# Kernel tuning notes

Hardware: AMD Instinct MI355X
Metric: run time of the kernel (lower is better)

The kernel has to match this reference:

```python
import jax, jax.numpy as jnp
import numpy as np
from jax import lax

DIM = 384
NH = 8
HD = DIM // NH
M = 16          # num_anchors
B = 16
HH = 64
WW = 64
N = HH * WW
STD = 0.02


def setup_inputs() -> dict:
    key = jax.random.key(0)
    ks = jax.random.split(key, 12)
    rn = lambda k, shape: (jax.random.normal(k, shape, jnp.float32) * STD)
    return {
        "x": jax.random.normal(ks[0], (B, N, DIM), jnp.float32),
        "H": HH,
        "W": WW,
        "saliency_w": rn(ks[1], (DIM, 1)),
        "saliency_b": jnp.zeros((1,), jnp.float32),
        "anchor_seeds": rn(ks[2], (1, M, DIM)),
        "w_q_agg": rn(ks[3], (DIM, DIM)),
        "w_kv_agg": rn(ks[4], (DIM, 2 * DIM)),
        "w_q_self": rn(ks[5], (DIM, DIM)),
        "w_kv_self": rn(ks[6], (DIM, 2 * DIM)),
        "w_q_bcast": rn(ks[7], (DIM, DIM)),
        "w_kv_bcast": rn(ks[8], (DIM, 2 * DIM)),
        "dw_kernel": rn(ks[9], (DIM, 1, 3, 3)),  # depthwise conv, OIHW with I=1
        "w_proj": rn(ks[10], (DIM, DIM)),
    }


def _mhsa(q_in, kv_in, wq, wkv):
    """Multi-head cross attention. q_in: [B,Lq,C], kv_in: [B,Lk,C]."""
    b, lq, c = q_in.shape
    lk = kv_in.shape[1]
    scale = HD ** -0.5
    q = (q_in @ wq).reshape(b, lq, NH, HD)
    kv = (kv_in @ wkv).reshape(b, lk, 2, NH, HD)
    k, v = kv[:, :, 0], kv[:, :, 1]
    attn = jnp.einsum("bqhd,bkhd->bhqk", q, k) * scale
    attn = jax.nn.softmax(attn, axis=-1)
    out = jnp.einsum("bhqk,bkhd->bqhd", attn, v).reshape(b, lq, c)
    return out


def reference(x, H, W, saliency_w, saliency_b, anchor_seeds,
              w_q_agg, w_kv_agg, w_q_self, w_kv_self,
              w_q_bcast, w_kv_bcast, dw_kernel, w_proj):
    b, n, c = x.shape
    # saliency gating
    sal = jax.nn.sigmoid(x @ saliency_w + saliency_b)  # [B,N,1]
    x_sal = x * sal
    # stage 1: anchors aggregate from saliency-gated tokens
    anchors = jnp.broadcast_to(anchor_seeds, (b, M, c))
    anchors = anchors + _mhsa(anchors, x_sal, w_q_agg, w_kv_agg)
    # stage 2: anchor self-attention
    anchors = anchors + _mhsa(anchors, anchors, w_q_self, w_kv_self)
    # stage 3: broadcast anchors back to all tokens
    global_out = _mhsa(x, anchors, w_q_bcast, w_kv_bcast)
    # depthwise 3x3 conv on the 2D token map
    x2d = x.reshape(b, H, W, c).transpose(0, 3, 1, 2)  # NCHW
    local = lax.conv_general_dilated(
        x2d, dw_kernel, window_strides=(1, 1), padding="SAME",
        feature_group_count=c,
        dimension_numbers=("NCHW", "OIHW", "NCHW"))
    local = local.transpose(0, 2, 3, 1).reshape(b, n, c)
    return (global_out + local) @ w_proj
```

## Files before the change

### kernel.cpp

```cpp
#include <hip/hip_runtime.h>
#include <hip/hip_bf16.h>

#define SCALE 0.14433756729740643f

typedef __attribute__((ext_vector_type(8))) short bf16x8;
typedef __attribute__((ext_vector_type(4))) float f32x4;

template <typename T> __device__ inline T cvt_from_f(float v);
template <> __device__ inline float cvt_from_f<float>(float v) { return v; }
template <> __device__ inline __hip_bfloat16 cvt_from_f<__hip_bfloat16>(float v) { return __float2bfloat16(v); }

__device__ inline void gload16(const void* g, void* l) {
  __builtin_amdgcn_global_load_lds((const __attribute__((address_space(1))) void*)g,
                                   (__attribute__((address_space(3))) void*)l, 16, 0, 0);
}

__device__ inline int xcd_flat(int nwg) {
  int flat = (blockIdx.z * gridDim.y + blockIdx.y) * gridDim.x + blockIdx.x;
  int per = nwg >> 3;
  return (flat & 7) * per + (flat >> 3);
}

__global__ __launch_bounds__(256) void prep(const float* __restrict__ x,
                                            const float* __restrict__ wsal,
                                            const float* __restrict__ bsal,
                                            __hip_bfloat16* __restrict__ xb,
                                            float* __restrict__ sal) {
  int wave = threadIdx.x >> 6, lane = threadIdx.x & 63;
  size_t row = (size_t)blockIdx.x * 4 + wave;
  const float* xr = x + row * 384;
  float xs[6];
  float part = 0.f;
#pragma unroll
  for (int j = 0; j < 6; j++) {
    int c = lane + 64 * j;
    xs[j] = xr[c];
    part += xs[j] * wsal[c];
  }
#pragma unroll
  for (int off = 32; off >= 1; off >>= 1) part += __shfl_xor(part, off);
  float s = 1.f / (1.f + __expf(-(part + bsal[0])));
#pragma unroll
  for (int j = 0; j < 6; j++) {
    int c = lane + 64 * j;
    xb[row * 384 + c] = __float2bfloat16(xs[j]);
  }
  if (lane == 0) sal[row] = s;
}

__global__ void wcast_tv(const float* __restrict__ w, __hip_bfloat16* __restrict__ wt) {
  int idx = blockIdx.x * 256 + threadIdx.x;
  if (idx >= 384 * 384) return;
  int n = idx / 384, k = idx % 384;
  wt[idx] = __float2bfloat16(w[(size_t)k * 768 + 384 + n]);
}

template <int K, typename OT, int BSHIFT>
__global__ __launch_bounds__(256) void gemm_mfma(const __hip_bfloat16* __restrict__ A,
                                                 const __hip_bfloat16* __restrict__ BT,
                                                 OT* __restrict__ out, int Ncols,
                                                 size_t btBatchStride) {
  __shared__ __align__(16) __hip_bfloat16 Asl[128][32];
  __shared__ __align__(16) __hip_bfloat16 Bsl[128][32];
  int nf = xcd_flat(gridDim.x * gridDim.y);
  int bX = nf % gridDim.x, bY = nf / gridDim.x;
  int tid = threadIdx.x;
  int lane = tid & 63;
  int w = tid >> 6;
  int wr = w >> 1, wc = w & 1;
  int fr = lane & 15, fq = lane >> 4;
  int rowBase = bY * 128, colBase = bX * 128;
  const __hip_bfloat16* BTb = BT + (size_t)(rowBase >> BSHIFT) * btBatchStride;

  int r1 = tid >> 2, kc1 = tid & 3;
  int r2 = (tid + 256) >> 2;

  char* aB1 = (char*)Asl + (size_t)(w * 64) * 16;
  char* aB2 = (char*)Asl + (size_t)(256 + w * 64) * 16;
  char* bB1 = (char*)Bsl + (size_t)(w * 64) * 16;
  char* bB2 = (char*)Bsl + (size_t)(256 + w * 64) * 16;

  const __hip_bfloat16* a1 = A + (size_t)(rowBase + r1) * K + kc1 * 8;
  const __hip_bfloat16* a2 = A + (size_t)(rowBase + r2) * K + kc1 * 8;
  const __hip_bfloat16* b1 = BTb + (size_t)(colBase + r1) * K + kc1 * 8;
  const __hip_bfloat16* b2 = BTb + (size_t)(colBase + r2) * K + kc1 * 8;

  f32x4 acc[4][4] = {};

  for (int kk = 0; kk < K; kk += 32) {
    gload16(a1 + kk, aB1);
    gload16(a2 + kk, aB2);
    gload16(b1 + kk, bB1);
    gload16(b2 + kk, bB2);
    __syncthreads();
    bf16x8 af[4], bfv[4];
#pragma unroll
    for (int m = 0; m < 4; m++) af[m] = *(const bf16x8*)&Asl[wr * 64 + m * 16 + fr][fq * 8];
#pragma unroll
    for (int n = 0; n < 4; n++) bfv[n] = *(const bf16x8*)&Bsl[wc * 64 + n * 16 + fr][fq * 8];
#pragma unroll
    for (int m = 0; m < 4; m++)
#pragma unroll
      for (int n = 0; n < 4; n++)
        acc[m][n] = __builtin_amdgcn_mfma_f32_16x16x32_bf16(af[m], bfv[n], acc[m][n], 0, 0, 0);
    __syncthreads();
  }

#pragma unroll
  for (int m = 0; m < 4; m++) {
    int row0 = rowBase + wr * 64 + m * 16 + fq * 4;
#pragma unroll
    for (int n = 0; n < 4; n++) {
      int col = colBase + wc * 64 + n * 16 + fr;
      f32x4 v = acc[m][n];
#pragma unroll
      for (int r = 0; r < 4; r++) out[(size_t)(row0 + r) * Ncols + col] = cvt_from_f<OT>(v[r]);
    }
  }
}

__global__ __launch_bounds__(256) void gemm_vlog(const __hip_bfloat16* __restrict__ A,
                                                 const __hip_bfloat16* __restrict__ BT,
                                                 __hip_bfloat16* __restrict__ vT,
                                                 float* __restrict__ lgT,
                                                 const float* __restrict__ rowScale) {
  constexpr int K = 384;
  __shared__ __align__(16) __hip_bfloat16 Asl[128][32];
  __shared__ __align__(16) __hip_bfloat16 Bsl[128][32];
  int nf = xcd_flat(2048);
  int bX = nf & 3, bY = nf >> 2;
  int tid = threadIdx.x;
  int lane = tid & 63;
  int w = tid >> 6;
  int wr = w >> 1, wc = w & 1;
  int fr = lane & 15, fq = lane >> 4;
  int rowBase = bY * 128, colBase = bX * 128;

  int r1 = tid >> 2, kc1 = tid & 3;
  int r2 = (tid + 256) >> 2;

  char* aB1 = (char*)Asl + (size_t)(w * 64) * 16;
  char* aB2 = (char*)Asl + (size_t)(256 + w * 64) * 16;
  char* bB1 = (char*)Bsl + (size_t)(w * 64) * 16;
  char* bB2 = (char*)Bsl + (size_t)(256 + w * 64) * 16;

  const __hip_bfloat16* a1 = A + (size_t)(rowBase + r1) * K + kc1 * 8;
  const __hip_bfloat16* a2 = A + (size_t)(rowBase + r2) * K + kc1 * 8;
  const __hip_bfloat16* b1 = BT + (size_t)(colBase + r1) * K + kc1 * 8;
  const __hip_bfloat16* b2 = BT + (size_t)(colBase + r2) * K + kc1 * 8;

  f32x4 acc[4][4] = {};

  for (int kk = 0; kk < K; kk += 32) {
    gload16(a1 + kk, aB1);
    gload16(a2 + kk, aB2);
    gload16(b1 + kk, bB1);
    gload16(b2 + kk, bB2);
    __syncthreads();
    bf16x8 af[4], bfv[4];
#pragma unroll
    for (int m = 0; m < 4; m++) af[m] = *(const bf16x8*)&Asl[wr * 64 + m * 16 + fr][fq * 8];
#pragma unroll
    for (int n = 0; n < 4; n++) bfv[n] = *(const bf16x8*)&Bsl[wc * 64 + n * 16 + fr][fq * 8];
#pragma unroll
    for (int m = 0; m < 4; m++)
#pragma unroll
      for (int n = 0; n < 4; n++)
        acc[m][n] = __builtin_amdgcn_mfma_f32_16x16x32_bf16(af[m], bfv[n], acc[m][n], 0, 0, 0);
    __syncthreads();
  }

  float sv[4][4];
#pragma unroll
  for (int m = 0; m < 4; m++)
#pragma unroll
    for (int r = 0; r < 4; r++)
      sv[m][r] = rowScale[rowBase + wr * 64 + m * 16 + fq * 4 + r];

  if (bX < 3) {
#pragma unroll
    for (int m = 0; m < 4; m++) {
      int row0 = rowBase + wr * 64 + m * 16 + fq * 4;
      int bb = row0 >> 12;
      int n0 = row0 & 4095;
#pragma unroll
      for (int n = 0; n < 4; n++) {
        int col = colBase + wc * 64 + n * 16 + fr;
        __hip_bfloat16 tb[4];
#pragma unroll
        for (int r = 0; r < 4; r++) tb[r] = __float2bfloat16(acc[m][n][r] * sv[m][r]);
        *(unsigned long long*)(vT + ((size_t)bb * 384 + col) * 4096 + n0) = *(unsigned long long*)tb;
      }
    }
  } else {
#pragma unroll
    for (int m = 0; m < 4; m++) {
      int row0 = rowBase + wr * 64 + m * 16 + fq * 4;
      int bb = row0 >> 12;
      int n0 = row0 & 4095;
#pragma unroll
      for (int n = 0; n < 4; n++) {
        int col = wc * 64 + n * 16 + fr;
        float4 v;
        v.x = acc[m][n][0] * sv[m][0];
        v.y = acc[m][n][1] * sv[m][1];
        v.z = acc[m][n][2] * sv[m][2];
        v.w = acc[m][n][3] * sv[m][3];
        *(float4*)(lgT + ((size_t)bb * 128 + col) * 4096 + n0) = v;
      }
    }
  }
}

__global__ __launch_bounds__(256) void gemm_pv(const __hip_bfloat16* __restrict__ PT,
                                               const __hip_bfloat16* __restrict__ vT,
                                               float* __restrict__ pbuf) {
  __shared__ __align__(16) __hip_bfloat16 Asl[128][32];
  __shared__ __align__(16) __hip_bfloat16 Bsl[128][32];
  int nf = xcd_flat(384);
  int bX = nf % 3, bY = (nf / 3) & 15, kz = nf / 48;
  int tid = threadIdx.x;
  int lane = tid & 63;
  int w = tid >> 6;
  int wr = w >> 1, wc = w & 1;
  int fr = lane & 15, fq = lane >> 4;
  int rowBase = bY * 128, colBase = bX * 128;
  const __hip_bfloat16* BTb = vT + (size_t)bY * 384 * 4096;

  int r1 = tid >> 2, kc1 = tid & 3;
  int r2 = (tid + 256) >> 2;

  char* aB1 = (char*)Asl + (size_t)(w * 64) * 16;
  char* aB2 = (char*)Asl + (size_t)(256 + w * 64) * 16;
  char* bB1 = (char*)Bsl + (size_t)(w * 64) * 16;
  char* bB2 = (char*)Bsl + (size_t)(256 + w * 64) * 16;

  const __hip_bfloat16* a1 = PT + (size_t)(rowBase + r1) * 4096 + kz * 512 + kc1 * 8;
  const __hip_bfloat16* a2 = PT + (size_t)(rowBase + r2) * 4096 + kz * 512 + kc1 * 8;
  const __hip_bfloat16* b1 = BTb + (size_t)(colBase + r1) * 4096 + kz * 512 + kc1 * 8;
  const __hip_bfloat16* b2 = BTb + (size_t)(colBase + r2) * 4096 + kz * 512 + kc1 * 8;

  f32x4 acc[4][4] = {};

  for (int kk = 0; kk < 512; kk += 32) {
    gload16(a1 + kk, aB1);
    gload16(a2 + kk, aB2);
    gload16(b1 + kk, bB1);
    gload16(b2 + kk, bB2);
    __syncthreads();
    bf16x8 af[4], bfv[4];
#pragma unroll
    for (int m = 0; m < 4; m++) af[m] = *(const bf16x8*)&Asl[wr * 64 + m * 16 + fr][fq * 8];
#pragma unroll
    for (int n = 0; n < 4; n++) bfv[n] = *(const bf16x8*)&Bsl[wc * 64 + n * 16 + fr][fq * 8];
#pragma unroll
    for (int m = 0; m < 4; m++)
#pragma unroll
      for (int n = 0; n < 4; n++)
        acc[m][n] = __builtin_amdgcn_mfma_f32_16x16x32_bf16(af[m], bfv[n], acc[m][n], 0, 0, 0);
    __syncthreads();
  }

  float* outz = pbuf + (size_t)kz * 786432;
#pragma unroll
  for (int m = 0; m < 4; m++) {
    int row0 = rowBase + wr * 64 + m * 16 + fq * 4;
#pragma unroll
    for (int n = 0; n < 4; n++) {
      int col = colBase + wc * 64 + n * 16 + fr;
      f32x4 v = acc[m][n];
#pragma unroll
      for (int r = 0; r < 4; r++) outz[(size_t)(row0 + r) * 384 + col] = v[r];
    }
  }
}

__global__ void anch_fix2(const float* __restrict__ pbuf, const float* __restrict__ seeds,
                          float* __restrict__ anch1) {
  int idx = blockIdx.x * 256 + threadIdx.x;
  int b = idx / 6144;
  int rem = idx - b * 6144;
  int m = rem / 384, c = rem - m * 384;
  int g = b * 128 + (c / 48) * 16 + m;
  const float* p = pbuf + (size_t)g * 384 + c;
  float s = 0.f;
#pragma unroll
  for (int z = 0; z < 8; z++) s += p[(size_t)z * 786432];
  anch1[idx] = seeds[rem] + s;
}

__global__ __launch_bounds__(256) void softmax_rows(const float* __restrict__ lgT,
                                                    __hip_bfloat16* __restrict__ PT) {
  int g = blockIdx.x;
  const float* row = lgT + (size_t)g * 4096;
  int tid = threadIdx.x, wv = tid >> 6, lane = tid & 63;
  __shared__ float redm[4], reds[4];
  float v[16];
  const float4* rp = (const float4*)(row + tid * 16);
#pragma unroll
  for (int i = 0; i < 4; i++) {
    float4 q = rp[i];
    v[i * 4] = q.x; v[i * 4 + 1] = q.y; v[i * 4 + 2] = q.z; v[i * 4 + 3] = q.w;
  }
  float mx = v[0];
#pragma unroll
  for (int i = 1; i < 16; i++) mx = fmaxf(mx, v[i]);
#pragma unroll
  for (int off = 1; off < 64; off <<= 1) mx = fmaxf(mx, __shfl_xor(mx, off));
  if (lane == 0) redm[wv] = mx;
  __syncthreads();
  mx = fmaxf(fmaxf(redm[0], redm[1]), fmaxf(redm[2], redm[3]));
  float s = 0.f;
#pragma unroll
  for (int i = 0; i < 16; i++) {
    v[i] = __expf(v[i] - mx);
    s += v[i];
  }
#pragma unroll
  for (int off = 1; off < 64; off <<= 1) s += __shfl_xor(s, off);
  if (lane == 0) reds[wv] = s;
  __syncthreads();
  s = (reds[0] + reds[1]) + (reds[2] + reds[3]);
  float inv = 1.f / s;
  __hip_bfloat16 tb[16];
#pragma unroll
  for (int i = 0; i < 16; i++) tb[i] = __float2bfloat16(v[i] * inv);
  __hip_bfloat16* op = PT + (size_t)g * 4096 + tid * 16;
  *(ulonglong2*)op = *(ulonglong2*)tb;
  *(ulonglong2*)(op + 8) = *(ulonglong2*)(tb + 8);
}

__global__ void fill_wl(const float* __restrict__ wkv, const float* __restrict__ qseed,
                        __hip_bfloat16* __restrict__ wvlT) {
  int idx = blockIdx.x * 256 + threadIdx.x;
  int hm = idx / 384, ci = idx - hm * 384;
  int h = hm >> 4, m = hm & 15;
  const float* wp = wkv + (size_t)ci * 768 + h * 48;
  const float* qp = qseed + m * 384 + h * 48;
  float acc = 0.f;
#pragma unroll
  for (int d = 0; d < 48; d++) acc += wp[d] * qp[d];
  wvlT[384 * 384 + idx] = __float2bfloat16(acc);
}

__global__ __launch_bounds__(256) void pgemm(const __hip_bfloat16* __restrict__ A,
                                             const __hip_bfloat16* __restrict__ wpbT,
                                             __hip_bfloat16* __restrict__ A2) {
  constexpr int K = 384;
  __shared__ __align__(16) __hip_bfloat16 Asl[128][32];
  __shared__ __align__(16) __hip_bfloat16 Bsl[128][32];
  int tid = threadIdx.x;
  int lane = tid & 63;
  int w = tid >> 6;
  int wr = w >> 1, wc = w & 1;
  int fr = lane & 15, fq = lane >> 4;
  int rowBase = blockIdx.y * 128;
  const __hip_bfloat16* BTb = wpbT + (size_t)(rowBase >> 12) * (128 * 384);

  int r1 = tid >> 2, kc1 = tid & 3;
  int r2 = (tid + 256) >> 2;

  char* aB1 = (char*)Asl + (size_t)(w * 64) * 16;
  char* aB2 = (char*)Asl + (size_t)(256 + w * 64) * 16;
  char* bB1 = (char*)Bsl + (size_t)(w * 64) * 16;
  char* bB2 = (char*)Bsl + (size_t)(256 + w * 64) * 16;

  const __hip_bfloat16* a1 = A + (size_t)(rowBase + r1) * K + kc1 * 8;
  const __hip_bfloat16* a2 = A + (size_t)(rowBase + r2) * K + kc1 * 8;
  const __hip_bfloat16* b1 = BTb + (size_t)r1 * K + kc1 * 8;
  const __hip_bfloat16* b2 = BTb + (size_t)r2 * K + kc1 * 8;

  f32x4 acc[4][4] = {};

  for (int kk = 0; kk < K; kk += 32) {
    gload16(a1 + kk, aB1);
    gload16(a2 + kk, aB2);
    gload16(b1 + kk, bB1);
    gload16(b2 + kk, bB2);
    __syncthreads();
    bf16x8 af[4], bfv[4];
#pragma unroll
    for (int m = 0; m < 4; m++) af[m] = *(const bf16x8*)&Asl[wr * 64 + m * 16 + fr][fq * 8];
#pragma unroll
    for (int n = 0; n < 4; n++) bfv[n] = *(const bf16x8*)&Bsl[wc * 64 + n * 16 + fr][fq * 8];
#pragma unroll
    for (int m = 0; m < 4; m++)
#pragma unroll
      for (int n = 0; n < 4; n++)
        acc[m][n] = __builtin_amdgcn_mfma_f32_16x16x32_bf16(af[m], bfv[n], acc[m][n], 0, 0, 0);
    __syncthreads();
  }

#pragma unroll
  for (int m = 0; m < 4; m++) {
    int row0 = rowBase + wr * 64 + m * 16 + fq * 4;
#pragma unroll
    for (int n = 0; n < 4; n++) {
      int col = wc * 64 + n * 16 + fr;
      f32x4 v = acc[m][n];
      f32x4 mx = v;
#pragma unroll
      for (int off = 1; off < 16; off <<= 1)
#pragma unroll
        for (int r = 0; r < 4; r++) mx[r] = fmaxf(mx[r], __shfl_xor(mx[r], off));
      f32x4 e;
#pragma unroll
      for (int r = 0; r < 4; r++) e[r] = __expf(v[r] - mx[r]);
      f32x4 s = e;
#pragma unroll
      for (int off = 1; off < 16; off <<= 1)
#pragma unroll
        for (int r = 0; r < 4; r++) s[r] += __shfl_xor(s[r], off);
#pragma unroll
      for (int r = 0; r < 4; r++)
        A2[(size_t)(row0 + r) * 512 + 384 + col] = __float2bfloat16(e[r] / s[r]);
    }
  }
}

__global__ __launch_bounds__(256) void anchor_proj2(const float* __restrict__ A,
                                                    const float* __restrict__ W,
                                                    float* __restrict__ out, int wstride,
                                                    int scaleCols) {
  int cs = blockIdx.x * 16;
  int b = blockIdx.y;
  __shared__ float a1[16][385];
  int tid = threadIdx.x;
  for (int idx = tid; idx < 6144; idx += 256) a1[idx / 384][idx % 384] = A[b * 6144 + idx];
  __syncthreads();
  int m = tid >> 4, cc = tid & 15;
  int col = cs + cc;
  const float* wp = W + col;
  float acc0 = 0.f, acc1 = 0.f, acc2 = 0.f, acc3 = 0.f;
#pragma unroll 4
  for (int k = 0; k < 384; k += 4) {
    acc0 += a1[m][k] * wp[(size_t)k * wstride];
    acc1 += a1[m][k + 1] * wp[(size_t)(k + 1) * wstride];
    acc2 += a1[m][k + 2] * wp[(size_t)(k + 2) * wstride];
    acc3 += a1[m][k + 3] * wp[(size_t)(k + 3) * wstride];
  }
  float acc = (acc0 + acc1) + (acc2 + acc3);
  if (col < scaleCols) acc *= SCALE;
  out[((size_t)b * 16 + m) * wstride + col] = acc;
}

__global__ void self_attn(const float* __restrict__ qsf, const float* __restrict__ kvs,
                          const float* __restrict__ anch1, float* __restrict__ anch2) {
  int h = blockIdx.x & 7, b = blockIdx.x >> 3;
  __shared__ float qs[16][48], ks[16][48], vs[16][48], p[16][17];
  int tid = threadIdx.x;
  for (int idx = tid; idx < 768; idx += 256) {
    int m = idx / 48, d = idx % 48;
    qs[m][d] = qsf[(b * 16 + m) * 384 + h * 48 + d];
    ks[m][d] = kvs[(b * 16 + m) * 768 + h * 48 + d];
    vs[m][d] = kvs[(b * 16 + m) * 768 + 384 + h * 48 + d];
  }
  __syncthreads();
  {
    int mq = tid >> 4, mk = tid & 15;
    float acc = 0.f;
    for (int d = 0; d < 48; d++) acc += qs[mq][d] * ks[mk][d];
    p[mq][mk] = acc;
  }
  __syncthreads();
  if (tid < 16) {
    float mx = -1e30f;
    for (int mk = 0; mk < 16; mk++) mx = fmaxf(mx, p[tid][mk]);
    float sum = 0.f;
    for (int mk = 0; mk < 16; mk++) {
      float e = __expf(p[tid][mk] - mx);
      p[tid][mk] = e;
      sum += e;
    }
    float inv = 1.f / sum;
    for (int mk = 0; mk < 16; mk++) p[tid][mk] *= inv;
  }
  __syncthreads();
  for (int idx = tid; idx < 768; idx += 256) {
    int m = idx / 48, d = idx % 48;
    float acc = 0.f;
    for (int mk = 0; mk < 16; mk++) acc += p[m][mk] * vs[mk][d];
    int c = h * 48 + d;
    anch2[(b * 16 + m) * 384 + c] = anch1[(b * 16 + m) * 384 + c] + acc;
  }
}

__global__ void fill_wpb(const float* __restrict__ wq, const float* __restrict__ kvb,
                         __hip_bfloat16* __restrict__ wpbT) {
  int idx = blockIdx.x * 256 + threadIdx.x;
  int b = idx / 49152;
  int rem = idx - b * 49152;
  int hm = rem / 384, k = rem - hm * 384;
  int h = hm >> 4, m = hm & 15;
  const float* kp = kvb + ((size_t)(b * 16 + m)) * 768 + h * 48;
  const float* wp = wq + (size_t)k * 384 + h * 48;
  float acc = 0.f;
#pragma unroll
  for (int d = 0; d < 48; d++) acc += wp[d] * kp[d];
  wpbT[idx] = __float2bfloat16(acc);
}

__global__ void fill_bt2(const float* __restrict__ wproj, const float* __restrict__ kvb,
                         __hip_bfloat16* __restrict__ bt2) {
  int idx = blockIdx.x * 256 + threadIdx.x;
  int b = idx / 196608;
  int rem = idx - b * 196608;
  int cp = rem / 512, k2 = rem - cp * 512;
  float v;
  if (k2 < 384) {
    v = wproj[(size_t)k2 * 384 + cp];
  } else {
    int hm = k2 - 384, h = hm >> 4, m = hm & 15;
    const float* vp = kvb + ((size_t)(b * 16 + m)) * 768 + 384 + h * 48;
    const float* wp2 = wproj + (size_t)(h * 48) * 384 + cp;
    v = 0.f;
#pragma unroll
    for (int d = 0; d < 48; d++) v += vp[d] * wp2[(size_t)d * 384];
  }
  bt2[idx] = __float2bfloat16(v);
}

__global__ __launch_bounds__(256) void dwconv2(const __hip_bfloat16* __restrict__ xb,
                                               const float* __restrict__ dwk,
                                               __hip_bfloat16* __restrict__ A2) {
  int b = blockIdx.y;
  int wv = threadIdx.x >> 6, lane = threadIdx.x & 63;
  int c0 = lane * 6;
  float kw[6][9];
#pragma unroll
  for (int i = 0; i < 6; i++)
#pragma unroll
    for (int ki = 0; ki < 9; ki++) kw[i][ki] = dwk[(c0 + i) * 9 + ki];
  for (int it = 0; it < 8; it++) {
    int p = blockIdx.x * 32 + wv * 8 + it;
    int y = p >> 6, w = p & 63;
    size_t prow = (size_t)b * 4096 + p;
    float acc[6] = {};
#pragma unroll
    for (int dy = -1; dy <= 1; dy++) {
      int yy = y + dy;
      if (yy < 0 || yy >= 64) continue;
#pragma unroll
      for (int dx = -1; dx <= 1; dx++) {
        int ww = w + dx;
        if (ww < 0 || ww >= 64) continue;
        int ki = (dy + 1) * 3 + (dx + 1);
        const __hip_bfloat16* xp = xb + ((size_t)(b * 4096 + yy * 64 + ww)) * 384 + c0;
#pragma unroll
        for (int i = 0; i < 6; i++) acc[i] += __bfloat162float(xp[i]) * kw[i][ki];
      }
    }
    __hip_bfloat16 tb[6];
#pragma unroll
    for (int i = 0; i < 6; i++) tb[i] = __float2bfloat16(acc[i]);
    __hip_bfloat16* gp = A2 + prow * 512 + c0;
    *(unsigned int*)(gp) = *(unsigned int*)(tb);
    *(unsigned int*)(gp + 2) = *(unsigned int*)(tb + 2);
    *(unsigned int*)(gp + 4) = *(unsigned int*)(tb + 4);
  }
}

extern "C" void kernel_launch(void* const* d_in, const int* in_sizes, int n_in,
                              void* d_out, int out_size, void* d_ws, size_t ws_size,
                              hipStream_t stream) {
  (void)in_sizes; (void)n_in; (void)out_size; (void)ws_size;
  const float* x = (const float*)d_in[0];
  const float* wsal = (const float*)d_in[3];
  const float* bsal = (const float*)d_in[4];
  const float* seeds = (const float*)d_in[5];
  const float* w_q_agg = (const float*)d_in[6];
  const float* w_kv_agg = (const float*)d_in[7];
  const float* w_q_self = (const float*)d_in[8];
  const float* w_kv_self = (const float*)d_in[9];
  const float* w_q_bcast = (const float*)d_in[10];
  const float* w_kv_bcast = (const float*)d_in[11];
  const float* dwk = (const float*)d_in[12];
  const float* w_proj = (const float*)d_in[13];
  float* out = (float*)d_out;

  char* ws = (char*)d_ws;
  size_t off = 0;
  auto take = [&](size_t bytes) -> void* {
    void* p = ws + off;
    off += (bytes + 255) & ~(size_t)255;
    return p;
  };
  __hip_bfloat16* xb = (__hip_bfloat16*)take(50331648);
  __hip_bfloat16* vT = (__hip_bfloat16*)take(50331648);
  float* logitsT = (float*)take(33554432);
  __hip_bfloat16* PT = (__hip_bfloat16*)take(16777216);
  float* qseed = (float*)take(24576);
  float* sal = (float*)take(262144);
  float* anch1 = (float*)take(393216);
  float* anch2 = (float*)take(393216);
  float* q_self = (float*)take(393216);
  float* kv_self = (float*)take(786432);
  float* kv_b = (float*)take(786432);
  __hip_bfloat16* wvlT = (__hip_bfloat16*)take(393216);
  __hip_bfloat16* wpbT = (__hip_bfloat16*)take(1572864);
  __hip_bfloat16* bt2 = (__hip_bfloat16*)take(6291456);
  float* pbuf = logitsT;
  __hip_bfloat16* A2 = vT;

  prep<<<16384, 256, 0, stream>>>(x, wsal, bsal, xb, sal);
  anchor_proj2<<<dim3(24, 1), 256, 0, stream>>>(seeds, w_q_agg, qseed, 384, 384);
  wcast_tv<<<576, 256, 0, stream>>>(w_kv_agg, wvlT);
  fill_wl<<<192, 256, 0, stream>>>(w_kv_agg, qseed, wvlT);
  gemm_vlog<<<dim3(4, 512), 256, 0, stream>>>(xb, wvlT, vT, logitsT, sal);
  softmax_rows<<<2048, 256, 0, stream>>>(logitsT, PT);
  gemm_pv<<<dim3(3, 16, 8), 256, 0, stream>>>(PT, vT, pbuf);
  anch_fix2<<<384, 256, 0, stream>>>(pbuf, seeds, anch1);
  anchor_proj2<<<dim3(24, 16), 256, 0, stream>>>(anch1, w_q_self, q_self, 384, 384);
  anchor_proj2<<<dim3(48, 16), 256, 0, stream>>>(anch1, w_kv_self, kv_self, 768, 0);
  self_attn<<<128, 256, 0, stream>>>(q_self, kv_self, anch1, anch2);
  anchor_proj2<<<dim3(48, 16), 256, 0, stream>>>(anch2, w_kv_bcast, kv_b, 768, 384);
  fill_wpb<<<3072, 256, 0, stream>>>(w_q_bcast, kv_b, wpbT);
  fill_bt2<<<12288, 256, 0, stream>>>(w_proj, kv_b, bt2);
  dwconv2<<<dim3(128, 16), 256, 0, stream>>>(xb, dwk, A2);
  pgemm<<<dim3(1, 512), 256, 0, stream>>>(xb, wpbT, A2);
  gemm_mfma<512, float, 12><<<dim3(3, 512), 256, 0, stream>>>(A2, bt2, out, 384, (size_t)384 * 512);
}
```

Baseline: 389.4 us.

## Store logits in bf16, fuse dwconv into pgemm, merge small launches

The stage-1 logits are now written and read as bf16 rather than fp32, which halves the traffic between gemm_vlog and softmax_rows. The depthwise 3x3 conv is folded into the tail of pgemm so each block also fills its own rows of A2, removing the separate dwconv launch. The q and kv self-projection launches are merged into one, as are fill_wpb and fill_bt2, to reduce launch overhead. The costs are lower precision in the softmax logits and a longer serial tail inside the pgemm blocks.

Result: faster. 373.0 us (-4.2%).

```diff
diff --git a/kernel.cpp b/kernel.cpp
--- a/kernel.cpp
+++ b/kernel.cpp
@@ -122,7 +122,7 @@
 __global__ __launch_bounds__(256) void gemm_vlog(const __hip_bfloat16* __restrict__ A,
                                                  const __hip_bfloat16* __restrict__ BT,
                                                  __hip_bfloat16* __restrict__ vT,
-                                                 float* __restrict__ lgT,
+                                                 __hip_bfloat16* __restrict__ lgT,
                                                  const float* __restrict__ rowScale) {
   constexpr int K = 384;
   __shared__ __align__(16) __hip_bfloat16 Asl[128][32];
@@ -201,12 +201,10 @@
 #pragma unroll
       for (int n = 0; n < 4; n++) {
         int col = wc * 64 + n * 16 + fr;
-        float4 v;
-        v.x = acc[m][n][0] * sv[m][0];
-        v.y = acc[m][n][1] * sv[m][1];
-        v.z = acc[m][n][2] * sv[m][2];
-        v.w = acc[m][n][3] * sv[m][3];
-        *(float4*)(lgT + ((size_t)bb * 128 + col) * 4096 + n0) = v;
+        __hip_bfloat16 tb[4];
+#pragma unroll
+        for (int r = 0; r < 4; r++) tb[r] = __float2bfloat16(acc[m][n][r] * sv[m][r]);
+        *(unsigned long long*)(lgT + ((size_t)bb * 128 + col) * 4096 + n0) = *(unsigned long long*)tb;
       }
     }
   }
@@ -289,18 +287,20 @@
   anch1[idx] = seeds[rem] + s;
 }
 
-__global__ __launch_bounds__(256) void softmax_rows(const float* __restrict__ lgT,
+__global__ __launch_bounds__(256) void softmax_rows(const __hip_bfloat16* __restrict__ lgT,
                                                     __hip_bfloat16* __restrict__ PT) {
   int g = blockIdx.x;
-  const float* row = lgT + (size_t)g * 4096;
+  const __hip_bfloat16* row = lgT + (size_t)g * 4096;
   int tid = threadIdx.x, wv = tid >> 6, lane = tid & 63;
   __shared__ float redm[4], reds[4];
   float v[16];
-  const float4* rp = (const float4*)(row + tid * 16);
-#pragma unroll
-  for (int i = 0; i < 4; i++) {
-    float4 q = rp[i];
-    v[i * 4] = q.x; v[i * 4 + 1] = q.y; v[i * 4 + 2] = q.z; v[i * 4 + 3] = q.w;
+  union { ulonglong2 u; __hip_bfloat16 h[8]; } L0, L1;
+  L0.u = *(const ulonglong2*)(row + tid * 16);
+  L1.u = *(const ulonglong2*)(row + tid * 16 + 8);
+#pragma unroll
+  for (int i = 0; i < 8; i++) {
+    v[i] = __bfloat162float(L0.h[i]);
+    v[8 + i] = __bfloat162float(L1.h[i]);
   }
   float mx = v[0];
 #pragma unroll
@@ -343,9 +343,10 @@
   wvlT[384 * 384 + idx] = __float2bfloat16(acc);
 }
 
-__global__ __launch_bounds__(256) void pgemm(const __hip_bfloat16* __restrict__ A,
-                                             const __hip_bfloat16* __restrict__ wpbT,
-                                             __hip_bfloat16* __restrict__ A2) {
+__global__ __launch_bounds__(256) void pgemm_conv(const __hip_bfloat16* __restrict__ A,
+                                                  const __hip_bfloat16* __restrict__ wpbT,
+                                                  const float* __restrict__ dwk,
+                                                  __hip_bfloat16* __restrict__ A2) {
   constexpr int K = 384;
   __shared__ __align__(16) __hip_bfloat16 Asl[128][32];
   __shared__ __align__(16) __hip_bfloat16 Bsl[128][32];
@@ -415,6 +416,42 @@
       for (int r = 0; r < 4; r++)
         A2[(size_t)(row0 + r) * 512 + 384 + col] = __float2bfloat16(e[r] / s[r]);
     }
+  }
+
+  int c0 = lane * 6;
+  float kw[6][9];
+#pragma unroll
+  for (int i = 0; i < 6; i++)
+#pragma unroll
+    for (int ki = 0; ki < 9; ki++) kw[i][ki] = dwk[(c0 + i) * 9 + ki];
+  int bb2 = rowBase >> 12;
+  int p0 = rowBase & 4095;
+  for (int it = 0; it < 32; it++) {
+    int p = p0 + w * 32 + it;
+    int y = p >> 6, wx = p & 63;
+    size_t prow = (size_t)rowBase + w * 32 + it;
+    float acc2[6] = {};
+#pragma unroll
+    for (int dy = -1; dy <= 1; dy++) {
+      int yy = y + dy;
+      if (yy < 0 || yy >= 64) continue;
+#pragma unroll
+      for (int dx = -1; dx <= 1; dx++) {
+        int ww2 = wx + dx;
+        if (ww2 < 0 || ww2 >= 64) continue;
+        int ki = (dy + 1) * 3 + (dx + 1);
+        const __hip_bfloat16* xp = A + ((size_t)(bb2 * 4096 + yy * 64 + ww2)) * 384 + c0;
+#pragma unroll
+        for (int i = 0; i < 6; i++) acc2[i] += __bfloat162float(xp[i]) * kw[i][ki];
+      }
+    }
+    __hip_bfloat16 tb[6];
+#pragma unroll
+    for (int i = 0; i < 6; i++) tb[i] = __float2bfloat16(acc2[i]);
+    __hip_bfloat16* gp = A2 + prow * 512 + c0;
+    *(unsigned int*)(gp) = *(unsigned int*)(tb);
+    *(unsigned int*)(gp + 2) = *(unsigned int*)(tb + 2);
+    *(unsigned int*)(gp + 4) = *(unsigned int*)(tb + 4);
   }
 }
 
@@ -444,6 +481,38 @@
   out[((size_t)b * 16 + m) * wstride + col] = acc;
 }
 
+__global__ __launch_bounds__(256) void anchor_proj_qkv(const float* __restrict__ A,
+                                                       const float* __restrict__ Wq,
+                                                       const float* __restrict__ Wkv,
+                                                       float* __restrict__ q_out,
+                                                       float* __restrict__ kv_out) {
+  bool isQ = blockIdx.x < 24;
+  int bx = isQ ? blockIdx.x : blockIdx.x - 24;
+  const float* W = isQ ? Wq : Wkv;
+  float* outp = isQ ? q_out : kv_out;
+  int wstride = isQ ? 384 : 768;
+  float scale = isQ ? SCALE : 1.f;
+  int cs = bx * 16;
+  int b = blockIdx.y;
+  __shared__ float a1[16][385];
+  int tid = threadIdx.x;
+  for (int idx = tid; idx < 6144; idx += 256) a1[idx / 384][idx % 384] = A[b * 6144 + idx];
+  __syncthreads();
+  int m = tid >> 4, cc = tid & 15;
+  int col = cs + cc;
+  const float* wp = W + col;
+  float acc0 = 0.f, acc1 = 0.f, acc2 = 0.f, acc3 = 0.f;
+#pragma unroll 4
+  for (int k = 0; k < 384; k += 4) {
+    acc0 += a1[m][k] * wp[(size_t)k * wstride];
+    acc1 += a1[m][k + 1] * wp[(size_t)(k + 1) * wstride];
+    acc2 += a1[m][k + 2] * wp[(size_t)(k + 2) * wstride];
+    acc3 += a1[m][k + 3] * wp[(size_t)(k + 3) * wstride];
+  }
+  float acc = ((acc0 + acc1) + (acc2 + acc3)) * scale;
+  outp[((size_t)b * 16 + m) * wstride + col] = acc;
+}
+
 __global__ void self_attn(const float* __restrict__ qsf, const float* __restrict__ kvs,
                           const float* __restrict__ anch1, float* __restrict__ anch2) {
   int h = blockIdx.x & 7, b = blockIdx.x >> 3;
@@ -485,78 +554,39 @@
   }
 }
 
-__global__ void fill_wpb(const float* __restrict__ wq, const float* __restrict__ kvb,
-                         __hip_bfloat16* __restrict__ wpbT) {
+__global__ void fill_wb(const float* __restrict__ wq, const float* __restrict__ wproj,
+                        const float* __restrict__ kvb,
+                        __hip_bfloat16* __restrict__ wpbT,
+                        __hip_bfloat16* __restrict__ bt2) {
   int idx = blockIdx.x * 256 + threadIdx.x;
-  int b = idx / 49152;
-  int rem = idx - b * 49152;
-  int hm = rem / 384, k = rem - hm * 384;
-  int h = hm >> 4, m = hm & 15;
-  const float* kp = kvb + ((size_t)(b * 16 + m)) * 768 + h * 48;
-  const float* wp = wq + (size_t)k * 384 + h * 48;
-  float acc = 0.f;
-#pragma unroll
-  for (int d = 0; d < 48; d++) acc += wp[d] * kp[d];
-  wpbT[idx] = __float2bfloat16(acc);
-}
-
-__global__ void fill_bt2(const float* __restrict__ wproj, const float* __restrict__ kvb,
-                         __hip_bfloat16* __restrict__ bt2) {
-  int idx = blockIdx.x * 256 + threadIdx.x;
-  int b = idx / 196608;
-  int rem = idx - b * 196608;
-  int cp = rem / 512, k2 = rem - cp * 512;
-  float v;
-  if (k2 < 384) {
-    v = wproj[(size_t)k2 * 384 + cp];
+  if (idx < 786432) {
+    int b = idx / 49152;
+    int rem = idx - b * 49152;
+    int hm = rem / 384, k = rem - hm * 384;
+    int h = hm >> 4, m = hm & 15;
+    const float* kp = kvb + ((size_t)(b * 16 + m)) * 768 + h * 48;
+    const float* wp = wq + (size_t)k * 384 + h * 48;
+    float acc = 0.f;
+#pragma unroll
+    for (int d = 0; d < 48; d++) acc += wp[d] * kp[d];
+    wpbT[idx] = __float2bfloat16(acc);
   } else {
-    int hm = k2 - 384, h = hm >> 4, m = hm & 15;
-    const float* vp = kvb + ((size_t)(b * 16 + m)) * 768 + 384 + h * 48;
-    const float* wp2 = wproj + (size_t)(h * 48) * 384 + cp;
-    v = 0.f;
-#pragma unroll
-    for (int d = 0; d < 48; d++) v += vp[d] * wp2[(size_t)d * 384];
-  }
-  bt2[idx] = __float2bfloat16(v);
-}
-
-__global__ __launch_bounds__(256) void dwconv2(const __hip_bfloat16* __restrict__ xb,
-                                               const float* __restrict__ dwk,
-                                               __hip_bfloat16* __restrict__ A2) {
-  int b = blockIdx.y;
-  int wv = threadIdx.x >> 6, lane = threadIdx.x & 63;
-  int c0 = lane * 6;
-  float kw[6][9];
-#pragma unroll
-  for (int i = 0; i < 6; i++)
-#pragma unroll
-    for (int ki = 0; ki < 9; ki++) kw[i][ki] = dwk[(c0 + i) * 9 + ki];
-  for (int it = 0; it < 8; it++) {
-    int p = blockIdx.x * 32 + wv * 8 + it;
-    int y = p >> 6, w = p & 63;
-    size_t prow = (size_t)b * 4096 + p;
-    float acc[6] = {};
-#pragma unroll
-    for (int dy = -1; dy <= 1; dy++) {
-      int yy = y + dy;
-      if (yy < 0 || yy >= 64) continue;
-#pragma unroll
-      for (int dx = -1; dx <= 1; dx++) {
-        int ww = w + dx;
-        if (ww < 0 || ww >= 64) continue;
-        int ki = (dy + 1) * 3 + (dx + 1);
-        const __hip_bfloat16* xp = xb + ((size_t)(b * 4096 + yy * 64 + ww)) * 384 + c0;
-#pragma unroll
-        for (int i = 0; i < 6; i++) acc[i] += __bfloat162float(xp[i]) * kw[i][ki];
-      }
-    }
-    __hip_bfloat16 tb[6];
-#pragma unroll
-    for (int i = 0; i < 6; i++) tb[i] = __float2bfloat16(acc[i]);
-    __hip_bfloat16* gp = A2 + prow * 512 + c0;
-    *(unsigned int*)(gp) = *(unsigned int*)(tb);
-    *(unsigned int*)(gp + 2) = *(unsigned int*)(tb + 2);
-    *(unsigned int*)(gp + 4) = *(unsigned int*)(tb + 4);
+    int j = idx - 786432;
+    int b = j / 196608;
+    int rem = j - b * 196608;
+    int cp = rem / 512, k2 = rem - cp * 512;
+    float v;
+    if (k2 < 384) {
+      v = wproj[(size_t)k2 * 384 + cp];
+    } else {
+      int hm = k2 - 384, h = hm >> 4, m = hm & 15;
+      const float* vp = kvb + ((size_t)(b * 16 + m)) * 768 + 384 + h * 48;
+      const float* wp2 = wproj + (size_t)(h * 48) * 384 + cp;
+      v = 0.f;
+#pragma unroll
+      for (int d = 0; d < 48; d++) v += vp[d] * wp2[(size_t)d * 384];
+    }
+    bt2[j] = __float2bfloat16(v);
   }
 }
 
@@ -587,7 +617,7 @@
   };
   __hip_bfloat16* xb = (__hip_bfloat16*)take(50331648);
   __hip_bfloat16* vT = (__hip_bfloat16*)take(50331648);
-  float* logitsT = (float*)take(33554432);
+  char* lgRegion = (char*)take(33554432);
   __hip_bfloat16* PT = (__hip_bfloat16*)take(16777216);
   float* qseed = (float*)take(24576);
   float* sal = (float*)take(262144);
@@ -599,7 +629,8 @@
   __hip_bfloat16* wvlT = (__hip_bfloat16*)take(393216);
   __hip_bfloat16* wpbT = (__hip_bfloat16*)take(1572864);
   __hip_bfloat16* bt2 = (__hip_bfloat16*)take(6291456);
-  float* pbuf = logitsT;
+  __hip_bfloat16* logitsT = (__hip_bfloat16*)lgRegion;
+  float* pbuf = (float*)lgRegion;
   __hip_bfloat16* A2 = vT;
 
   prep<<<16384, 256, 0, stream>>>(x, wsal, bsal, xb, sal);
@@ -610,13 +641,10 @@
   softmax_rows<<<2048, 256, 0, stream>>>(logitsT, PT);
   gemm_pv<<<dim3(3, 16, 8), 256, 0, stream>>>(PT, vT, pbuf);
   anch_fix2<<<384, 256, 0, stream>>>(pbuf, seeds, anch1);
-  anchor_proj2<<<dim3(24, 16), 256, 0, stream>>>(anch1, w_q_self, q_self, 384, 384);
-  anchor_proj2<<<dim3(48, 16), 256, 0, stream>>>(anch1, w_kv_self, kv_self, 768, 0);
+  anchor_proj_qkv<<<dim3(72, 16), 256, 0, stream>>>(anch1, w_q_self, w_kv_self, q_self, kv_self);
   self_attn<<<128, 256, 0, stream>>>(q_self, kv_self, anch1, anch2);
   anchor_proj2<<<dim3(48, 16), 256, 0, stream>>>(anch2, w_kv_bcast, kv_b, 768, 384);
-  fill_wpb<<<3072, 256, 0, stream>>>(w_q_bcast, kv_b, wpbT);
-  fill_bt2<<<12288, 256, 0, stream>>>(w_proj, kv_b, bt2);
-  dwconv2<<<dim3(128, 16), 256, 0, stream>>>(xb, dwk, A2);
-  pgemm<<<dim3(1, 512), 256, 0, stream>>>(xb, wpbT, A2);
+  fill_wb<<<15360, 256, 0, stream>>>(w_q_bcast, w_proj, kv_b, wpbT, bt2);
+  pgemm_conv<<<dim3(1, 512), 256, 0, stream>>>(xb, wpbT, dwk, A2);
   gemm_mfma<512, float, 12><<<dim3(3, 512), 256, 0, stream>>>(A2, bt2, out, 384, (size_t)384 * 512);
 }
```
